# Kernel tuning notes

Measured on AMD Instinct MI355X. Metric: run time of the kernel, lower is better.

The kernel has to match this reference:

```python
import jax, jax.numpy as jnp
import numpy as np

B, T, D = 4, 2048, 1024
N_HEADS = 16
D_HEAD = D // N_HEADS


def setup_inputs() -> dict:
    key = jax.random.key(0)
    ks = jax.random.split(key, 5)
    s = 1.0 / np.sqrt(D)  # keep activations well-scaled
    return {
        "x": jax.random.normal(ks[0], (B, T, D), dtype=jnp.float32),
        "Wq": jax.random.normal(ks[1], (D, D), dtype=jnp.float32) * s,
        "Wk": jax.random.normal(ks[2], (D, D), dtype=jnp.float32) * s,
        "Wv": jax.random.normal(ks[3], (D, D), dtype=jnp.float32) * s,
        "Wo": jax.random.normal(ks[4], (D, D), dtype=jnp.float32) * s,
    }


def reference(x, Wq, Wk, Wv, Wo):
    Bx, Tx, C = x.shape
    # projections; nn.Linear(d,d,bias=False): y = x @ W^T
    def split_heads(y):
        return y.reshape(Bx, Tx, N_HEADS, D_HEAD).transpose(0, 2, 1, 3)  # [B,H,T,dh]
    q = split_heads(x @ Wq.T)
    k = split_heads(x @ Wk.T)
    v = split_heads(x @ Wv.T)
    scale = 1.0 / np.sqrt(D_HEAD)
    att = jnp.einsum("bhtd,bhsd->bhts", q, k) * scale  # [B,H,T,T]
    causal = jnp.tril(jnp.ones((Tx, Tx), dtype=bool))
    att = jnp.where(causal[None, None], att, -jnp.inf)
    att = jax.nn.softmax(att, axis=-1)
    y = jnp.einsum("bhts,bhsd->bhtd", att, v)  # [B,H,T,dh]
    y = y.transpose(0, 2, 1, 3).reshape(Bx, Tx, C)
    return y @ Wo.T
```

## Files before the change

kernel.cpp:

```cpp
#include <hip/hip_runtime.h>
#include <cstdint>
#include <cstddef>

typedef unsigned short u16;
typedef short bf16x8 __attribute__((ext_vector_type(8)));
typedef unsigned short u16x8 __attribute__((ext_vector_type(8)));
typedef float f32x4 __attribute__((ext_vector_type(4)));
typedef float f32x16 __attribute__((ext_vector_type(16)));
typedef unsigned u32x2 __attribute__((ext_vector_type(2)));

__device__ __forceinline__ u16 f2bf(float x) {
    union { float f; unsigned int u; } v; v.f = x;
    unsigned int u = v.u;
    unsigned int r = (u + 0x7fffu + ((u >> 16) & 1u)) >> 16;
    return (u16)r;
}

__device__ __forceinline__ unsigned cvtpk(float lo, float hi) {
    unsigned r;
    asm("v_cvt_pk_bf16_f32 %0, %1, %2" : "=v"(r) : "v"(lo), "v"(hi));
    return r;
}

__device__ __forceinline__ float exp2v(float x) {
    float y;
    asm("v_exp_f32 %0, %1" : "=v"(y) : "v"(x));
    return y;
}

__device__ __forceinline__ void load_lds16(const void* g, void* l) {
    __builtin_amdgcn_global_load_lds((const __attribute__((address_space(1))) void*)g,
                                     (__attribute__((address_space(3))) void*)l, 16, 0, 0);
}

__global__ void cast_f32_bf16(const float* __restrict__ in, u16* __restrict__ out, int n) {
    int i = (blockIdx.x * blockDim.x + threadIdx.x) * 4;
    int stride = gridDim.x * blockDim.x * 4;
    for (; i < n; i += stride) {
        float4 f = *reinterpret_cast<const float4*>(in + i);
        ushort4 o;
        o.x = f2bf(f.x); o.y = f2bf(f.y); o.z = f2bf(f.z); o.w = f2bf(f.w);
        *reinterpret_cast<ushort4*>(out + i) = o;
    }
}

__global__ void cast_w4(const float* __restrict__ w0, const float* __restrict__ w1,
                        const float* __restrict__ w2, const float* __restrict__ w3,
                        u16* __restrict__ out, int nw) {
    const int wsel = blockIdx.y;
    const float* in = (wsel == 0) ? w0 : (wsel == 1) ? w1 : (wsel == 2) ? w2 : w3;
    u16* o = out + (size_t)wsel * nw;
    int i = (blockIdx.x * blockDim.x + threadIdx.x) * 4;
    int stride = gridDim.x * blockDim.x * 4;
    for (; i < nw; i += stride) {
        float4 f = *reinterpret_cast<const float4*>(in + i);
        ushort4 v;
        v.x = f2bf(f.x); v.y = f2bf(f.y); v.z = f2bf(f.z); v.w = f2bf(f.w);
        *reinterpret_cast<ushort4*>(o + i) = v;
    }
}

template <int MODE>
__global__ __launch_bounds__(256) void gemm_bt(const u16* __restrict__ A,
                                               const u16* __restrict__ Bw,
                                               void* __restrict__ outp,
                                               u16* __restrict__ vtg,
                                               int M, int N, int K) {
    __shared__ u16 smem[16384];
    u16* As = smem;
    u16* Bs = smem + 4096;

    const int tid  = threadIdx.x;
    const int m0   = blockIdx.x * 128;
    const int n0   = blockIdx.y * 128;
    const int wid  = tid >> 6;
    const int lane = tid & 63;
    const int wr   = (wid >> 1) * 64;
    const int wc   = (wid & 1) * 64;
    const int fr   = lane & 15;
    const int ko   = (lane >> 4) * 8;
    const int rq   = (lane >> 4) * 4;

    f32x4 acc[4][4];
#pragma unroll
    for (int i = 0; i < 4; ++i)
#pragma unroll
        for (int j = 0; j < 4; ++j) acc[i][j] = f32x4{0.f, 0.f, 0.f, 0.f};

    const int lr4 = lane >> 2;
    const int ls  = lane & 3;

    for (int k0 = 0; k0 < K; k0 += 32) {
#pragma unroll
        for (int t = 0; t < 2; ++t) {
            const int qtr = wid * 2 + t;
            const int r   = qtr * 16 + lr4;
            load_lds16(&A[(size_t)(m0 + r) * K + k0 + ls * 8], &As[qtr * 512]);
            load_lds16(&Bw[(size_t)(n0 + r) * K + k0 + ls * 8], &Bs[qtr * 512]);
        }
        __syncthreads();

        bf16x8 af[4], bfr[4];
#pragma unroll
        for (int mf = 0; mf < 4; ++mf)
            af[mf] = *reinterpret_cast<const bf16x8*>(&As[(wr + mf * 16 + fr) * 32 + ko]);
#pragma unroll
        for (int nf = 0; nf < 4; ++nf)
            bfr[nf] = *reinterpret_cast<const bf16x8*>(&Bs[(wc + nf * 16 + fr) * 32 + ko]);
        __builtin_amdgcn_s_setprio(1);
#pragma unroll
        for (int mf = 0; mf < 4; ++mf)
#pragma unroll
            for (int nf = 0; nf < 4; ++nf)
                acc[mf][nf] = __builtin_amdgcn_mfma_f32_16x16x32_bf16(
                    af[mf], bfr[nf], acc[mf][nf], 0, 0, 0);
        __builtin_amdgcn_s_setprio(0);
        __syncthreads();
    }

    if constexpr (MODE == 0) {
        float* C = (float*)outp;
#pragma unroll
        for (int mf = 0; mf < 4; ++mf)
#pragma unroll
            for (int nf = 0; nf < 4; ++nf)
#pragma unroll
                for (int i = 0; i < 4; ++i)
                    C[(size_t)(m0 + wr + mf * 16 + rq + i) * N + n0 + wc + nf * 16 + fr] =
                        acc[mf][nf][i];
    } else {
        if (n0 < 2048) {
            const float osc = (n0 < 1024) ? 0.18033688011112042f : 1.0f;
            u16* qk = (u16*)outp;
#pragma unroll
            for (int mf = 0; mf < 4; ++mf)
#pragma unroll
                for (int nf = 0; nf < 4; ++nf)
#pragma unroll
                    for (int i = 0; i < 4; ++i)
                        qk[(size_t)(m0 + wr + mf * 16 + rq + i) * 2048 + n0 + wc + nf * 16 + fr] =
                            f2bf(acc[mf][nf][i] * osc);
        } else {
#pragma unroll
            for (int mf = 0; mf < 4; ++mf)
#pragma unroll
                for (int nf = 0; nf < 4; ++nf)
#pragma unroll
                    for (int i = 0; i < 4; ++i) {
                        const int nl = wc + nf * 16 + fr;
                        const int ml = wr + mf * 16 + rq + i;
                        smem[nl * 128 + ((((ml * 2) ^ ((nl & 15) << 4))) >> 1)] =
                            f2bf(acc[mf][nf][i]);
                    }
            __syncthreads();
            const int bb   = m0 >> 11;
            const int tloc = m0 & 2047;
#pragma unroll
            for (int p = 0; p < 8; ++p) {
                const int nl = (tid >> 4) + p * 16;
                const int sl = tid & 15;
                u16x8 v = *reinterpret_cast<const u16x8*>(
                    &smem[nl * 128 + ((((sl * 16) ^ ((nl & 15) << 4))) >> 1)]);
                *reinterpret_cast<u16x8*>(
                    &vtg[(size_t)(bb * 1024 + (n0 - 2048) + nl) * 2048 + tloc + sl * 8]) = v;
            }
        }
    }
}

__global__ __launch_bounds__(256) void attn_fwd(const u16* __restrict__ qk,
                                                const u16* __restrict__ vtg,
                                                u16* __restrict__ Y) {
    constexpr int T = 2048, DQK = 2048, DOUT = 1024;
    const int jb = (int)blockIdx.y >> 3;
    const int bh = (int)blockIdx.x * 8 + ((int)blockIdx.y & 7);
    const int b  = bh >> 4, hd = bh & 15;
    const int tid = threadIdx.x, w = tid >> 6, lane = tid & 63;
    const int qloc = lane & 31, h2 = lane >> 5;

    __shared__ u16 Ks[2][4096];
    __shared__ u16 Vs[2][4096];

    const size_t rowb = (size_t)b * T;
    const int sr8 = lane >> 3, ss = lane & 7;

#define BUILD_PA(sv, RB, dst) {                                               \
        unsigned wa  = cvtpk(sv[RB + 0], sv[RB + 1]);                         \
        unsigned wb  = cvtpk(sv[RB + 2], sv[RB + 3]);                         \
        unsigned wc2 = cvtpk(sv[RB + 4], sv[RB + 5]);                         \
        unsigned wd  = cvtpk(sv[RB + 6], sv[RB + 7]);                         \
        u32x2 r0 = __builtin_amdgcn_permlane32_swap(wa, wc2, false, false);   \
        u32x2 r1 = __builtin_amdgcn_permlane32_swap(wb, wd, false, false);    \
        dst.x = r0.x; dst.y = r1.x; dst.z = r0.y; dst.w = r1.y; }

#define PV_STEP(pa, KS, ROWBASE, oacc) {                                      \
        const int rr_ = (ROWBASE) + qloc;                                     \
        bf16x8 vf_ = *reinterpret_cast<const bf16x8*>(                        \
            &Vb[rr_ * 64 + (((2 * (KS) + h2) ^ (rr_ & 7)) * 8)]);             \
        oacc = __builtin_amdgcn_mfma_f32_32x32x16_bf16(                       \
            *reinterpret_cast<const bf16x8*>(&pa), vf_, oacc, 0, 0, 0); }

    for (int qi = 0; qi < 2; ++qi) {
        const int qt = (qi == 0) ? (15 - jb) : jb;
        const int q0 = qt * 128;
        const int wq = q0 + w * 32;
        const int NT = 2 * qt + 2;

        bf16x8 qf[4];
#pragma unroll
        for (int ks = 0; ks < 4; ++ks)
            qf[ks] = *reinterpret_cast<const bf16x8*>(
                &qk[(rowb + wq + qloc) * DQK + hd * 64 + ks * 16 + h2 * 8]);

        f32x16 o0, o1;
#pragma unroll
        for (int i = 0; i < 16; ++i) { o0[i] = 0.f; o1[i] = 0.f; }
        float lp = 0.f;

        __syncthreads();

        {
            const int qtr = w * 2, r0 = qtr * 8 + sr8, r1 = r0 + 8;
            const int sc0 = (ss ^ (r0 & 7)) * 8, sc1 = (ss ^ (r1 & 7)) * 8;
            load_lds16(&qk[(rowb + r0) * DQK + 1024 + hd * 64 + sc0], &Ks[0][qtr * 512]);
            load_lds16(&vtg[((size_t)bh * 64 + r0) * T + sc0], &Vs[0][qtr * 512]);
            load_lds16(&qk[(rowb + r1) * DQK + 1024 + hd * 64 + sc1], &Ks[0][(qtr + 1) * 512]);
            load_lds16(&vtg[((size_t)bh * 64 + r1) * T + sc1], &Vs[0][(qtr + 1) * 512]);
        }

        for (int kt = 0; kt < NT; ++kt) {
            __syncthreads();

            if (kt + 1 < NT) {
                const int nb = (kt + 1) & 1;
                const int k0n = (kt + 1) * 64;
                const int qtr = w * 2, r0 = qtr * 8 + sr8, r1 = r0 + 8;
                const int sc0 = (ss ^ (r0 & 7)) * 8, sc1 = (ss ^ (r1 & 7)) * 8;
                load_lds16(&qk[(rowb + k0n + r0) * DQK + 1024 + hd * 64 + sc0], &Ks[nb][qtr * 512]);
                load_lds16(&vtg[((size_t)bh * 64 + r0) * T + k0n + sc0], &Vs[nb][qtr * 512]);
                load_lds16(&qk[(rowb + k0n + r1) * DQK + 1024 + hd * 64 + sc1], &Ks[nb][(qtr + 1) * 512]);
                load_lds16(&vtg[((size_t)bh * 64 + r1) * T + k0n + sc1], &Vs[nb][(qtr + 1) * 512]);
            }

            const int k0 = kt * 64;
            if (k0 <= wq + 31) {
                const u16* Kb = Ks[kt & 1];
                const u16* Vb = Vs[kt & 1];
                const bool do1 = (k0 + 32 <= wq + 31);
                const bool dm  = (k0 + 63 > wq);

                f32x16 st0, st1;
#pragma unroll
                for (int i = 0; i < 16; ++i) { st0[i] = 0.f; st1[i] = 0.f; }

                __builtin_amdgcn_s_setprio(1);
#pragma unroll
                for (int ks = 0; ks < 4; ++ks) {
                    bf16x8 kf = *reinterpret_cast<const bf16x8*>(
                        &Kb[qloc * 64 + (((2 * ks + h2) ^ (qloc & 7)) * 8)]);
                    st0 = __builtin_amdgcn_mfma_f32_32x32x16_bf16(kf, qf[ks], st0, 0, 0, 0);
                }
                if (do1) {
#pragma unroll
                    for (int ks = 0; ks < 4; ++ks) {
                        const int r1 = 32 + qloc;
                        bf16x8 kf = *reinterpret_cast<const bf16x8*>(
                            &Kb[r1 * 64 + (((2 * ks + h2) ^ (r1 & 7)) * 8)]);
                        st1 = __builtin_amdgcn_mfma_f32_32x32x16_bf16(kf, qf[ks], st1, 0, 0, 0);
                    }
                }
                __builtin_amdgcn_s_setprio(0);

                const int qg = wq + qloc;
#pragma unroll
                for (int i = 0; i < 16; ++i) st0[i] = exp2v(st0[i]);
                if (do1) {
#pragma unroll
                    for (int i = 0; i < 16; ++i) st1[i] = exp2v(st1[i]);
                }
                if (dm) {
#pragma unroll
                    for (int r = 0; r < 16; ++r) {
                        const int crow = (r & 3) + 8 * (r >> 2) + 4 * h2;
                        if (k0 + crow > qg)      st0[r] = 0.f;
                        if (k0 + 32 + crow > qg) st1[r] = 0.f;
                    }
                }
                {
                    float l0 = 0.f, l1 = 0.f, l2 = 0.f, l3 = 0.f;
#pragma unroll
                    for (int i = 0; i < 4; ++i) {
                        l0 += st0[i]; l1 += st0[4 + i]; l2 += st0[8 + i]; l3 += st0[12 + i];
                    }
                    if (do1) {
#pragma unroll
                        for (int i = 0; i < 4; ++i) {
                            l0 += st1[i]; l1 += st1[4 + i]; l2 += st1[8 + i]; l3 += st1[12 + i];
                        }
                    }
                    lp += (l0 + l1) + (l2 + l3);
                }

                uint4 pa0, pa1, pa2, pa3;
                BUILD_PA(st0, 0, pa0);
                BUILD_PA(st0, 8, pa1);
                if (do1) {
                    BUILD_PA(st1, 0, pa2);
                    BUILD_PA(st1, 8, pa3);
                }

                __builtin_amdgcn_s_setprio(1);
                PV_STEP(pa0, 0, 0, o0);
                PV_STEP(pa1, 1, 0, o0);
                PV_STEP(pa0, 0, 32, o1);
                PV_STEP(pa1, 1, 32, o1);
                if (do1) {
                    PV_STEP(pa2, 2, 0, o0);
                    PV_STEP(pa3, 3, 0, o0);
                    PV_STEP(pa2, 2, 32, o1);
                    PV_STEP(pa3, 3, 32, o1);
                }
                __builtin_amdgcn_s_setprio(0);
            }
        }

        const float lf = lp + __shfl_xor(lp, 32);
        const float linv = 1.0f / lf;
#pragma unroll
        for (int r = 0; r < 16; ++r) {
            const int crow = (r & 3) + 8 * (r >> 2) + 4 * h2;
            const float rl = __shfl(linv, crow);
            const size_t yrow = rowb + wq + crow;
            Y[yrow * DOUT + hd * 64 + qloc]      = (u16)cvtpk(o0[r] * rl, 0.f);
            Y[yrow * DOUT + hd * 64 + 32 + qloc] = (u16)cvtpk(o1[r] * rl, 0.f);
        }
    }
#undef BUILD_PA
#undef PV_STEP
}

extern "C" void kernel_launch(void* const* d_in, const int* in_sizes, int n_in,
                              void* d_out, int out_size, void* d_ws, size_t ws_size,
                              hipStream_t stream) {
    const float* x  = (const float*)d_in[0];
    const float* Wq = (const float*)d_in[1];
    const float* Wk = (const float*)d_in[2];
    const float* Wv = (const float*)d_in[3];
    const float* Wo = (const float*)d_in[4];

    constexpr int B = 4, T = 2048, D = 1024;
    constexpr int M = B * T;
    const int nx = in_sizes[0];
    const int nw = in_sizes[1];

    char* ws = (char*)d_ws;
    u16* xb   = (u16*)(ws);
    u16* qkb  = (u16*)(ws + (16ull << 20));
    u16* vtg  = (u16*)(ws + (48ull << 20));
    u16* yb   = (u16*)(ws + (64ull << 20));
    u16* wqkv = (u16*)(ws + (80ull << 20));
    u16* wob  = wqkv + 3 * (size_t)nw;

    cast_f32_bf16<<<2048, 256, 0, stream>>>(x, xb, nx);
    cast_w4<<<dim3(256, 4), 256, 0, stream>>>(Wq, Wk, Wv, Wo, wqkv, nw);

    gemm_bt<1><<<dim3(M / 128, 3072 / 128), 256, 0, stream>>>(xb, wqkv, qkb, vtg, M, 3072, D);

    attn_fwd<<<dim3(8, 64), 256, 0, stream>>>(qkb, vtg, yb);

    gemm_bt<0><<<dim3(M / 128, D / 128), 256, 0, stream>>>(yb, wob, d_out, nullptr, M, D, D);
}
```

Measured before the change: 168.5 us.

## Shrink attention blocks to 64 query rows with two waves and precomputed load pointers

The attention kernel now uses 128-thread blocks covering 64-row query tiles. Each block pairs tiles jb and 31-jb for causal balance, and the grid becomes 64x16 over batch-heads and tile pairs. K/V tile loads walk precomputed per-lane pointers, so each wave issues four chunk loads per tile. Separately, the V-transpose epilogue of the QKV GEMM packs four bf16 values into one 8-byte LDS store. The smaller blocks give more of them per CU, at the cost of more total K/V traffic and more syncs per query row.

New measurement: 179.2 us. +6.3%, slower.

```diff
diff --git a/kernel.cpp b/kernel.cpp
--- a/kernel.cpp
+++ b/kernel.cpp
@@ -144,14 +144,15 @@
 #pragma unroll
             for (int mf = 0; mf < 4; ++mf)
 #pragma unroll
-                for (int nf = 0; nf < 4; ++nf)
-#pragma unroll
-                    for (int i = 0; i < 4; ++i) {
-                        const int nl = wc + nf * 16 + fr;
-                        const int ml = wr + mf * 16 + rq + i;
-                        smem[nl * 128 + ((((ml * 2) ^ ((nl & 15) << 4))) >> 1)] =
-                            f2bf(acc[mf][nf][i]);
-                    }
+                for (int nf = 0; nf < 4; ++nf) {
+                    const int nl  = wc + nf * 16 + fr;
+                    const int ml0 = wr + mf * 16 + rq;
+                    uint2 pk;
+                    pk.x = cvtpk(acc[mf][nf][0], acc[mf][nf][1]);
+                    pk.y = cvtpk(acc[mf][nf][2], acc[mf][nf][3]);
+                    *reinterpret_cast<uint2*>(
+                        &smem[nl * 128 + ((((ml0 * 2) ^ ((nl & 15) << 4))) >> 1)]) = pk;
+                }
             __syncthreads();
             const int bb   = m0 >> 11;
             const int tloc = m0 & 2047;
@@ -168,12 +169,12 @@
     }
 }
 
-__global__ __launch_bounds__(256) void attn_fwd(const u16* __restrict__ qk,
+__global__ __launch_bounds__(128) void attn_fwd(const u16* __restrict__ qk,
                                                 const u16* __restrict__ vtg,
                                                 u16* __restrict__ Y) {
     constexpr int T = 2048, DQK = 2048, DOUT = 1024;
-    const int jb = (int)blockIdx.y >> 3;
-    const int bh = (int)blockIdx.x * 8 + ((int)blockIdx.y & 7);
+    const int bh = blockIdx.x;
+    const int jb = blockIdx.y;
     const int b  = bh >> 4, hd = bh & 15;
     const int tid = threadIdx.x, w = tid >> 6, lane = tid & 63;
     const int qloc = lane & 31, h2 = lane >> 5;
@@ -183,6 +184,7 @@
 
     const size_t rowb = (size_t)b * T;
     const int sr8 = lane >> 3, ss = lane & 7;
+    const int sc = (ss ^ sr8) * 8;
 
 #define BUILD_PA(sv, RB, dst) {                                               \
         unsigned wa  = cvtpk(sv[RB + 0], sv[RB + 1]);                         \
@@ -201,10 +203,10 @@
             *reinterpret_cast<const bf16x8*>(&pa), vf_, oacc, 0, 0, 0); }
 
     for (int qi = 0; qi < 2; ++qi) {
-        const int qt = (qi == 0) ? (15 - jb) : jb;
-        const int q0 = qt * 128;
+        const int qt = (qi == 0) ? (31 - jb) : jb;
+        const int q0 = qt * 64;
         const int wq = q0 + w * 32;
-        const int NT = 2 * qt + 2;
+        const int NT = qt + 1;
 
         bf16x8 qf[4];
 #pragma unroll
@@ -217,29 +219,39 @@
         for (int i = 0; i < 16; ++i) { o0[i] = 0.f; o1[i] = 0.f; }
         float lp = 0.f;
 
+        const u16* kp[4];
+        const u16* vp[4];
+#pragma unroll
+        for (int t = 0; t < 4; ++t) {
+            const int r = (w * 4 + t) * 8 + sr8;
+            kp[t] = qk + (rowb + r) * DQK + 1024 + hd * 64 + sc;
+            vp[t] = vtg + ((size_t)bh * 64 + r) * T + sc;
+        }
+
         __syncthreads();
 
-        {
-            const int qtr = w * 2, r0 = qtr * 8 + sr8, r1 = r0 + 8;
-            const int sc0 = (ss ^ (r0 & 7)) * 8, sc1 = (ss ^ (r1 & 7)) * 8;
-            load_lds16(&qk[(rowb + r0) * DQK + 1024 + hd * 64 + sc0], &Ks[0][qtr * 512]);
-            load_lds16(&vtg[((size_t)bh * 64 + r0) * T + sc0], &Vs[0][qtr * 512]);
-            load_lds16(&qk[(rowb + r1) * DQK + 1024 + hd * 64 + sc1], &Ks[0][(qtr + 1) * 512]);
-            load_lds16(&vtg[((size_t)bh * 64 + r1) * T + sc1], &Vs[0][(qtr + 1) * 512]);
-        }
+#pragma unroll
+        for (int t = 0; t < 4; ++t) {
+            const int chunk = w * 4 + t;
+            load_lds16(kp[t], &Ks[0][chunk * 512]);
+            load_lds16(vp[t], &Vs[0][chunk * 512]);
+        }
+#pragma unroll
+        for (int t = 0; t < 4; ++t) { kp[t] += 64 * DQK; vp[t] += 64; }
 
         for (int kt = 0; kt < NT; ++kt) {
             __syncthreads();
 
             if (kt + 1 < NT) {
                 const int nb = (kt + 1) & 1;
-                const int k0n = (kt + 1) * 64;
-                const int qtr = w * 2, r0 = qtr * 8 + sr8, r1 = r0 + 8;
-                const int sc0 = (ss ^ (r0 & 7)) * 8, sc1 = (ss ^ (r1 & 7)) * 8;
-                load_lds16(&qk[(rowb + k0n + r0) * DQK + 1024 + hd * 64 + sc0], &Ks[nb][qtr * 512]);
-                load_lds16(&vtg[((size_t)bh * 64 + r0) * T + k0n + sc0], &Vs[nb][qtr * 512]);
-                load_lds16(&qk[(rowb + k0n + r1) * DQK + 1024 + hd * 64 + sc1], &Ks[nb][(qtr + 1) * 512]);
-                load_lds16(&vtg[((size_t)bh * 64 + r1) * T + k0n + sc1], &Vs[nb][(qtr + 1) * 512]);
+#pragma unroll
+                for (int t = 0; t < 4; ++t) {
+                    const int chunk = w * 4 + t;
+                    load_lds16(kp[t], &Ks[nb][chunk * 512]);
+                    load_lds16(vp[t], &Vs[nb][chunk * 512]);
+                }
+#pragma unroll
+                for (int t = 0; t < 4; ++t) { kp[t] += 64 * DQK; vp[t] += 64; }
             }
 
             const int k0 = kt * 64;
@@ -366,7 +378,7 @@
 
     gemm_bt<1><<<dim3(M / 128, 3072 / 128), 256, 0, stream>>>(xb, wqkv, qkb, vtg, M, 3072, D);
 
-    attn_fwd<<<dim3(8, 64), 256, 0, stream>>>(qkb, vtg, yb);
+    attn_fwd<<<dim3(64, 16), 128, 0, stream>>>(qkb, vtg, yb);
 
     gemm_bt<0><<<dim3(M / 128, D / 128), 256, 0, stream>>>(yb, wob, d_out, nullptr, M, D, D);
 }
```
